# Performance work log

Hardware: AMD Instinct MI355X
Metric: run time of the kernel (lower is better)

Reference implementation:

```python
import jax, jax.numpy as jnp
import numpy as np

B, L, D_MODEL, N_HEAD = 8, 1024, 1024, 16
D_K = D_MODEL // N_HEAD  # 64


def setup_inputs() -> dict:
    key = jax.random.key(0)
    ks = jax.random.split(key, 10)
    scale = 1.0 / np.sqrt(D_MODEL)
    inp = {
        "q": jax.random.normal(ks[0], (B, L, D_MODEL), jnp.float32),
        "k": jax.random.normal(ks[1], (B, L, D_MODEL), jnp.float32),
        "v": jax.random.normal(ks[2], (B, L, D_MODEL), jnp.float32),
        "mask": jax.random.randint(ks[3], (B, L, L), 0, 2, jnp.int32),
        # per-head projection weights stacked: [H, d_model, d_k]
        "Wq": jax.random.normal(ks[4], (N_HEAD, D_MODEL, D_K), jnp.float32) * scale,
        "Wk": jax.random.normal(ks[5], (N_HEAD, D_MODEL, D_K), jnp.float32) * scale,
        "Wv": jax.random.normal(ks[6], (N_HEAD, D_MODEL, D_K), jnp.float32) * scale,
        # output projection (Dense with bias): [d_model, d_model], [d_model]
        "Wo": jax.random.normal(ks[7], (D_MODEL, D_MODEL), jnp.float32) * scale,
        "bo": jnp.zeros((D_MODEL,), jnp.float32),
    }
    return inp


def reference(q, k, v, mask, Wq, Wk, Wv, Wo, bo):
    d_k = Wq.shape[-1]
    # per-head projections (mode=1 per-head Dense, no bias), vectorized over heads
    qs = jnp.einsum('bld,hdk->bhlk', q, Wq)  # [B,H,Lq,d_k]
    ks = jnp.einsum('bld,hdk->bhlk', k, Wk)  # [B,H,Lk,d_k]
    vs = jnp.einsum('bld,hdk->bhlk', v, Wv)  # [B,H,Lk,d_v]
    # scaled dot-product attention: batch_dot(q,k,axes=[2,2]) / sqrt(d_k)
    scores = jnp.einsum('bhqd,bhkd->bhqk', qs, ks) / jnp.sqrt(jnp.float32(d_k))
    # additive mask: -1e9 * (1 - mask), broadcast over heads
    scores = scores + (-1e9 * (1.0 - mask.astype(jnp.float32)))[:, None, :, :]
    attn = jax.nn.softmax(scores, axis=-1)           # [B,H,Lq,Lk] (dropout inactive at inference)
    head = jnp.einsum('bhqk,bhkd->bhqd', attn, vs)   # [B,H,Lq,d_v]
    b, h, lq, dv = head.shape
    # Concatenate heads along feature axis (head index major, as in mode=1 Concatenate)
    head_cat = head.transpose(0, 2, 1, 3).reshape(b, lq, h * dv)
    outputs = head_cat @ Wo + bo                     # [B,Lq,d_model] (dropout inactive)
    # attn heads also concatenated along last axis in mode=1
    attn_cat = attn.transpose(0, 2, 1, 3).reshape(b, lq, h * attn.shape[-1])
    return outputs, attn_cat
```

## Files before the change

### kernel.cpp

```cpp
#include <hip/hip_runtime.h>

typedef _Float16 f16;
typedef _Float16 f16x8 __attribute__((ext_vector_type(8)));
typedef _Float16 f16x4 __attribute__((ext_vector_type(4)));
typedef float f32x4 __attribute__((ext_vector_type(4)));

#define GLOAD_LDS16(g, l) \
    __builtin_amdgcn_global_load_lds((const __attribute__((address_space(1))) void*)(g), \
                                     (__attribute__((address_space(3))) void*)(l), 16, 0, 0)

#define SC_LOG2E 0.180336880f

__global__ __launch_bounds__(256) void cvt3_kernel(const float* __restrict__ q,
        const float* __restrict__ k, const float* __restrict__ v, f16* __restrict__ out) {
    const int z = blockIdx.y;
    const float* src = (z == 0) ? q : (z == 1) ? k : v;
    const size_t i = ((size_t)blockIdx.x * 256 + threadIdx.x) * 8;
    float4 a = *(const float4*)&src[i], b2 = *(const float4*)&src[i + 4];
    f16x8 h;
    h[0] = (f16)a.x; h[1] = (f16)a.y; h[2] = (f16)a.z; h[3] = (f16)a.w;
    h[4] = (f16)b2.x; h[5] = (f16)b2.y; h[6] = (f16)b2.z; h[7] = (f16)b2.w;
    *(f16x8*)&out[(size_t)z * 8388608 + i] = h;
}

__global__ void transpose_w_kernel(const float* __restrict__ Wq, const float* __restrict__ Wk,
        const float* __restrict__ Wv, const float* __restrict__ Wo, f16* __restrict__ out) {
    const int z = blockIdx.y;
    int t = blockIdx.x * 256 + threadIdx.x;
    int n = t >> 10, d = t & 1023;
    float val;
    if (z < 3) {
        const float* W = (z == 0) ? Wq : (z == 1) ? Wk : Wv;
        val = W[((size_t)(n >> 6) * 1024 + d) * 64 + (n & 63)];
    } else {
        val = Wo[(size_t)d * 1024 + n];
    }
    out[(size_t)z * 1048576 + (size_t)n * 1024 + d] = (f16)val;
}

__global__ void maskbits_kernel(const int* __restrict__ mask, unsigned* __restrict__ bits) {
    int t = blockIdx.x * 256 + threadIdx.x;
    const int4* src = (const int4*)mask + (size_t)t * 8;
    unsigned w = 0;
#pragma unroll
    for (int i = 0; i < 8; ++i) {
        int4 v = src[i];
        w |= (v.x != 0 ? 1u : 0u) << (i * 4 + 0);
        w |= (v.y != 0 ? 1u : 0u) << (i * 4 + 1);
        w |= (v.z != 0 ? 1u : 0u) << (i * 4 + 2);
        w |= (v.w != 0 ? 1u : 0u) << (i * 4 + 3);
    }
    bits[t] = w;
}

__global__ __launch_bounds__(256) void proj_kernel(const f16* __restrict__ Ah,
        const f16* __restrict__ Wt, f16* __restrict__ Outp) {
    __shared__ __align__(16) f16 As[128][64];
    __shared__ __align__(16) f16 Bs[128][64];
    const int id = blockIdx.x;
    const int z = id >> 9;
    const int id2 = id & 511;
    const int m0 = ((id2 & 7) * 8 + ((id2 >> 3) & 7)) * 128;
    const int n0 = (id2 >> 6) * 128;
    const f16* A = Ah + (size_t)z * 8388608;
    const f16* Bt = Wt + (size_t)z * 1048576;
    f16* Out = Outp + (size_t)z * 8388608;
    const int tid = threadIdx.x, lane = tid & 63;
    const int w = tid >> 6, wr = w >> 1, wc = w & 1;

    f32x4 acc[4][4];
#pragma unroll
    for (int mi = 0; mi < 4; ++mi)
#pragma unroll
        for (int ni = 0; ni < 4; ++ni) acc[mi][ni] = (f32x4){0.f, 0.f, 0.f, 0.f};

    for (int kt = 0; kt < 16; ++kt) {
        const int k0 = kt * 64;
#pragma unroll
        for (int seg = 0; seg < 4; ++seg) {
            const int ch = seg * 256 + tid, r = ch >> 3, c = ch & 7;
            GLOAD_LDS16(&A[(size_t)(m0 + r) * 1024 + k0 + (c ^ (r & 7)) * 8],
                        (char*)&As[0][0] + (seg * 256 + w * 64) * 16);
            GLOAD_LDS16(&Bt[(size_t)(n0 + r) * 1024 + k0 + (c ^ (r & 7)) * 8],
                        (char*)&Bs[0][0] + (seg * 256 + w * 64) * 16);
        }
        __syncthreads();
#pragma unroll
        for (int ks = 0; ks < 2; ++ks) {
            const int slot = ks * 4 + (lane >> 4);
            f16x8 af[4], bf[4];
#pragma unroll
            for (int mi = 0; mi < 4; ++mi) {
                const int row = wr * 64 + mi * 16 + (lane & 15);
                af[mi] = *(const f16x8*)&As[row][(slot ^ (row & 7)) * 8];
            }
#pragma unroll
            for (int ni = 0; ni < 4; ++ni) {
                const int row = wc * 64 + ni * 16 + (lane & 15);
                bf[ni] = *(const f16x8*)&Bs[row][(slot ^ (row & 7)) * 8];
            }
#pragma unroll
            for (int mi = 0; mi < 4; ++mi)
#pragma unroll
                for (int ni = 0; ni < 4; ++ni)
                    acc[mi][ni] = __builtin_amdgcn_mfma_f32_16x16x32_f16(af[mi], bf[ni], acc[mi][ni], 0, 0, 0);
        }
        __syncthreads();
    }

    const float sc = (z == 0) ? SC_LOG2E : 1.0f;
#pragma unroll
    for (int mi = 0; mi < 4; ++mi)
#pragma unroll
        for (int ni = 0; ni < 4; ++ni) {
            const int row0 = m0 + wr * 64 + mi * 16 + ((lane >> 4) << 2);
            const int col = n0 + wc * 64 + ni * 16 + (lane & 15);
            const int h = col >> 6, kk = col & 63;
            const int b = row0 >> 10, l0 = row0 & 1023;
            if (z < 2) {
#pragma unroll
                for (int r = 0; r < 4; ++r)
                    Out[(((size_t)(b * 16 + h) * 1024) + l0 + r) * 64 + kk] = (f16)(acc[mi][ni][r] * sc);
            } else {
                f16x4 hv;
#pragma unroll
                for (int r = 0; r < 4; ++r) hv[r] = (f16)acc[mi][ni][r];
                *(f16x4*)&Out[((size_t)(b * 16 + h) * 64 + kk) * 1024 + l0] = hv;
            }
        }
}

__global__ __launch_bounds__(256) void out_kernel(const f16* __restrict__ A,
        const f16* __restrict__ Bt, float* __restrict__ O, const float* __restrict__ bias) {
    __shared__ __align__(16) f16 As[128][64];
    __shared__ __align__(16) f16 Bs[128][64];
    const int id2 = blockIdx.x;
    const int m0 = ((id2 & 7) * 8 + ((id2 >> 3) & 7)) * 128;
    const int n0 = (id2 >> 6) * 128;
    const int tid = threadIdx.x, lane = tid & 63;
    const int w = tid >> 6, wr = w >> 1, wc = w & 1;

    f32x4 acc[4][4];
#pragma unroll
    for (int mi = 0; mi < 4; ++mi)
#pragma unroll
        for (int ni = 0; ni < 4; ++ni) acc[mi][ni] = (f32x4){0.f, 0.f, 0.f, 0.f};

    for (int kt = 0; kt < 16; ++kt) {
        const int k0 = kt * 64;
#pragma unroll
        for (int seg = 0; seg < 4; ++seg) {
            const int ch = seg * 256 + tid, r = ch >> 3, c = ch & 7;
            GLOAD_LDS16(&A[(size_t)(m0 + r) * 1024 + k0 + (c ^ (r & 7)) * 8],
                        (char*)&As[0][0] + (seg * 256 + w * 64) * 16);
            GLOAD_LDS16(&Bt[(size_t)(n0 + r) * 1024 + k0 + (c ^ (r & 7)) * 8],
                        (char*)&Bs[0][0] + (seg * 256 + w * 64) * 16);
        }
        __syncthreads();
#pragma unroll
        for (int ks = 0; ks < 2; ++ks) {
            const int slot = ks * 4 + (lane >> 4);
            f16x8 af[4], bf[4];
#pragma unroll
            for (int mi = 0; mi < 4; ++mi) {
                const int row = wr * 64 + mi * 16 + (lane & 15);
                af[mi] = *(const f16x8*)&As[row][(slot ^ (row & 7)) * 8];
            }
#pragma unroll
            for (int ni = 0; ni < 4; ++ni) {
                const int row = wc * 64 + ni * 16 + (lane & 15);
                bf[ni] = *(const f16x8*)&Bs[row][(slot ^ (row & 7)) * 8];
            }
#pragma unroll
            for (int mi = 0; mi < 4; ++mi)
#pragma unroll
                for (int ni = 0; ni < 4; ++ni)
                    acc[mi][ni] = __builtin_amdgcn_mfma_f32_16x16x32_f16(af[mi], bf[ni], acc[mi][ni], 0, 0, 0);
        }
        __syncthreads();
    }

#pragma unroll
    for (int mi = 0; mi < 4; ++mi)
#pragma unroll
        for (int ni = 0; ni < 4; ++ni) {
            const int row0 = m0 + wr * 64 + mi * 16 + ((lane >> 4) << 2);
            const int col = n0 + wc * 64 + ni * 16 + (lane & 15);
            const float bb = bias[col];
#pragma unroll
            for (int r = 0; r < 4; ++r)
                __builtin_nontemporal_store(acc[mi][ni][r] + bb, &O[(size_t)(row0 + r) * 1024 + col]);
        }
}

__global__ __launch_bounds__(256) void attn_fused_kernel(const f16* __restrict__ Qp,
        const f16* __restrict__ Kp, const f16* __restrict__ VpT,
        const unsigned* __restrict__ bits, float* __restrict__ attn, f16* __restrict__ headcat) {
    __shared__ __align__(16) f16 Qs[128][64];
    __shared__ __align__(16) f16 Ks[2][64][64];
    __shared__ __align__(16) f16 Vs[2][64][64];
    __shared__ __align__(16) f16 Ps[128][64];
    __shared__ unsigned bm[128][32];
    const int bh = blockIdx.x & 127, m0 = (blockIdx.x >> 7) * 128;
    const int b = bh >> 4, h = bh & 15;
    const int tid = threadIdx.x, lane = tid & 63, w = tid >> 6;
    const f16* Qbase = Qp + (size_t)bh * 65536;
    const f16* Kbase = Kp + (size_t)bh * 65536;
    const f16* Vbase = VpT + (size_t)bh * 65536;

    auto stageK = [&](int buf, int j) {
#pragma unroll
        for (int seg = 0; seg < 2; ++seg) {
            const int ch = seg * 256 + tid, r = ch >> 3, c = ch & 7;
            GLOAD_LDS16(&Kbase[(size_t)(j * 64 + r) * 64 + (c ^ (r & 7)) * 8],
                        (char*)&Ks[buf][0][0] + (seg * 256 + w * 64) * 16);
        }
    };
    auto stageV = [&](int buf, int j) {
#pragma unroll
        for (int seg = 0; seg < 2; ++seg) {
            const int ch = seg * 256 + tid, r = ch >> 3, c = ch & 7;
            GLOAD_LDS16(&Vbase[(size_t)r * 1024 + j * 64 + (c ^ (r & 7)) * 8],
                        (char*)&Vs[buf][0][0] + (seg * 256 + w * 64) * 16);
        }
    };

#pragma unroll
    for (int seg = 0; seg < 4; ++seg) {
        const int ch = seg * 256 + tid, r = ch >> 3, c = ch & 7;
        GLOAD_LDS16(&Qbase[(size_t)(m0 + r) * 64 + (c ^ (r & 7)) * 8],
                    (char*)&Qs[0][0] + (seg * 256 + w * 64) * 16);
        GLOAD_LDS16((const char*)&bits[((size_t)b * 1024 + m0) * 32] + (size_t)(seg * 256 + tid) * 16,
                    (char*)&bm[0][0] + (seg * 256 + w * 64) * 16);
    }
    stageK(0, 0);
    __syncthreads();

    float lsum[2][4];
#pragma unroll
    for (int mi = 0; mi < 2; ++mi)
#pragma unroll
        for (int r = 0; r < 4; ++r) lsum[mi][r] = 0.f;

    for (int j = 0; j < 16; ++j) {
        if (j < 15) stageK((j + 1) & 1, j + 1);

        f32x4 acc[2][4];
#pragma unroll
        for (int mi = 0; mi < 2; ++mi)
#pragma unroll
            for (int ni = 0; ni < 4; ++ni) acc[mi][ni] = (f32x4){0.f, 0.f, 0.f, 0.f};
#pragma unroll
        for (int ks = 0; ks < 2; ++ks) {
            const int slot = ks * 4 + (lane >> 4);
            f16x8 af[2], bf[4];
#pragma unroll
            for (int mi = 0; mi < 2; ++mi) {
                const int row = w * 32 + mi * 16 + (lane & 15);
                af[mi] = *(const f16x8*)&Qs[row][(slot ^ (row & 7)) * 8];
            }
#pragma unroll
            for (int ni = 0; ni < 4; ++ni) {
                const int row = ni * 16 + (lane & 15);
                bf[ni] = *(const f16x8*)&Ks[j & 1][row][(slot ^ (row & 7)) * 8];
            }
#pragma unroll
            for (int mi = 0; mi < 2; ++mi)
#pragma unroll
                for (int ni = 0; ni < 4; ++ni)
                    acc[mi][ni] = __builtin_amdgcn_mfma_f32_16x16x32_f16(af[mi], bf[ni], acc[mi][ni], 0, 0, 0);
        }

#pragma unroll
        for (int mi = 0; mi < 2; ++mi)
#pragma unroll
            for (int r = 0; r < 4; ++r) {
                const int row = w * 32 + mi * 16 + ((lane >> 4) << 2) + r;
#pragma unroll
                for (int ni = 0; ni < 4; ++ni) {
                    const int col = j * 64 + ni * 16 + (lane & 15);
                    const float p = exp2f(acc[mi][ni][r]);
                    lsum[mi][r] += ((bm[row][col >> 5] >> (col & 31)) & 1) ? p : 0.f;
                }
            }
        __syncthreads();
    }

    stageK(0, 0);
    stageV(0, 0);

    float rl[2][4];
#pragma unroll
    for (int mi = 0; mi < 2; ++mi)
#pragma unroll
        for (int r = 0; r < 4; ++r) {
            float s = lsum[mi][r];
#pragma unroll
            for (int d = 1; d < 16; d <<= 1) s += __shfl_xor(s, d);
            rl[mi][r] = 1.0f / s;
        }

    f32x4 accP[2][4];
#pragma unroll
    for (int mi = 0; mi < 2; ++mi)
#pragma unroll
        for (int ni = 0; ni < 4; ++ni) accP[mi][ni] = (f32x4){0.f, 0.f, 0.f, 0.f};

    float* attnBase = attn + ((size_t)b * 1024 + m0) * 16384 + h * 1024;
    __syncthreads();

    const int st_r0 = tid >> 4;
    const int st_c4 = tid & 15;

    for (int j = 0; j < 16; ++j) {
        if (j < 15) { stageK((j + 1) & 1, j + 1); stageV((j + 1) & 1, j + 1); }

        f32x4 acc[2][4];
#pragma unroll
        for (int mi = 0; mi < 2; ++mi)
#pragma unroll
            for (int ni = 0; ni < 4; ++ni) acc[mi][ni] = (f32x4){0.f, 0.f, 0.f, 0.f};
#pragma unroll
        for (int ks = 0; ks < 2; ++ks) {
            const int slot = ks * 4 + (lane >> 4);
            f16x8 af[2], bf[4];
#pragma unroll
            for (int mi = 0; mi < 2; ++mi) {
                const int row = w * 32 + mi * 16 + (lane & 15);
                af[mi] = *(const f16x8*)&Qs[row][(slot ^ (row & 7)) * 8];
            }
#pragma unroll
            for (int ni = 0; ni < 4; ++ni) {
                const int row = ni * 16 + (lane & 15);
                bf[ni] = *(const f16x8*)&Ks[j & 1][row][(slot ^ (row & 7)) * 8];
            }
#pragma unroll
            for (int mi = 0; mi < 2; ++mi)
#pragma unroll
                for (int ni = 0; ni < 4; ++ni)
                    acc[mi][ni] = __builtin_amdgcn_mfma_f32_16x16x32_f16(af[mi], bf[ni], acc[mi][ni], 0, 0, 0);
        }

#pragma unroll
        for (int mi = 0; mi < 2; ++mi)
#pragma unroll
            for (int r = 0; r < 4; ++r) {
                const int row = w * 32 + mi * 16 + ((lane >> 4) << 2) + r;
                const float ll = rl[mi][r];
#pragma unroll
                for (int ni = 0; ni < 4; ++ni) {
                    const int col = j * 64 + ni * 16 + (lane & 15);
                    float p = exp2f(acc[mi][ni][r]) * ll;
                    p = ((bm[row][col >> 5] >> (col & 31)) & 1) ? p : 0.f;
                    Ps[row][(col & 63) ^ ((row & 7) << 3)] = (f16)p;
                }
            }
        __syncthreads();

#pragma unroll
        for (int i = 0; i < 8; ++i) {
            const int row = st_r0 + 16 * i;
            const f16x4 hv = *(const f16x4*)((const char*)&Ps[row][0] +
                    ((st_c4 >> 1) ^ (row & 7)) * 16 + (st_c4 & 1) * 8);
            f32x4 fv = {(float)hv[0], (float)hv[1], (float)hv[2], (float)hv[3]};
            __builtin_nontemporal_store(fv,
                    (f32x4*)&attnBase[(size_t)row * 16384 + j * 64 + st_c4 * 4]);
        }

#pragma unroll
        for (int ks = 0; ks < 2; ++ks) {
            const int slot = ks * 4 + (lane >> 4);
            f16x8 pf[2], vf[4];
#pragma unroll
            for (int mi = 0; mi < 2; ++mi) {
                const int row = w * 32 + mi * 16 + (lane & 15);
                pf[mi] = *(const f16x8*)&Ps[row][(slot ^ (row & 7)) * 8];
            }
#pragma unroll
            for (int ni = 0; ni < 4; ++ni) {
                const int row = ni * 16 + (lane & 15);
                vf[ni] = *(const f16x8*)&Vs[j & 1][row][(slot ^ (row & 7)) * 8];
            }
#pragma unroll
            for (int mi = 0; mi < 2; ++mi)
#pragma unroll
                for (int ni = 0; ni < 4; ++ni)
                    accP[mi][ni] = __builtin_amdgcn_mfma_f32_16x16x32_f16(pf[mi], vf[ni], accP[mi][ni], 0, 0, 0);
        }
        __syncthreads();
    }

#pragma unroll
    for (int mi = 0; mi < 2; ++mi)
#pragma unroll
        for (int ni = 0; ni < 4; ++ni) {
            const int row0 = m0 + w * 32 + mi * 16 + ((lane >> 4) << 2);
            const int col = ni * 16 + (lane & 15);
#pragma unroll
            for (int r = 0; r < 4; ++r)
                headcat[((size_t)b * 1024 + row0 + r) * 1024 + h * 64 + col] = (f16)accP[mi][ni][r];
        }
}

extern "C" void kernel_launch(void* const* d_in, const int* in_sizes, int n_in,
                              void* d_out, int out_size, void* d_ws, size_t ws_size,
                              hipStream_t stream) {
    const float* q = (const float*)d_in[0];
    const float* k = (const float*)d_in[1];
    const float* v = (const float*)d_in[2];
    const int* mask = (const int*)d_in[3];
    const float* Wq = (const float*)d_in[4];
    const float* Wk = (const float*)d_in[5];
    const float* Wv = (const float*)d_in[6];
    const float* Wo = (const float*)d_in[7];
    const float* bo = (const float*)d_in[8];

    float* out0 = (float*)d_out;
    float* attn = out0 + (size_t)8 * 1024 * 1024;

    char* ws = (char*)d_ws;
    f16* wt   = (f16*)(ws + ((size_t)0 << 20));
    f16* qh   = (f16*)(ws + ((size_t)8 << 20));
    f16* Qp   = (f16*)(ws + ((size_t)56 << 20));
    f16* Kp   = (f16*)(ws + ((size_t)72 << 20));
    f16* VpT  = (f16*)(ws + ((size_t)88 << 20));
    f16* hc   = (f16*)(ws + ((size_t)104 << 20));
    unsigned* bits = (unsigned*)(ws + ((size_t)120 << 20));
    f16* wot  = wt + (size_t)3 * 1048576;

    cvt3_kernel<<<dim3(4096, 3), 256, 0, stream>>>(q, k, v, qh);
    transpose_w_kernel<<<dim3(4096, 4), 256, 0, stream>>>(Wq, Wk, Wv, Wo, wt);
    maskbits_kernel<<<1024, 256, 0, stream>>>(mask, bits);

    proj_kernel<<<1536, 256, 0, stream>>>(qh, wt, Qp);

    attn_fused_kernel<<<1024, 256, 0, stream>>>(Qp, Kp, VpT, bits, attn, hc);

    out_kernel<<<512, 256, 0, stream>>>(hc, wot, out0, bo);
}
```

Measured before the change: 321.2 us.

## Transpose QK MFMA output, use mask-nibble LUTs and packed f16 softmax in attention

The QK^T MFMA operands are swapped so each lane holds four consecutive key columns of one query row. The mask can then be read as a 4-bit nibble from a swizzled bitmask word and expanded through small float/f16 lookup tables, replacing per-element bit tests. Row sums now need only two cross-lane shuffles instead of four per value. Normalisation and masking are done with packed f16 multiplies and written to LDS as 8-byte stores, and V is single-buffered and loaded each iteration. The PV MFMA is moved ahead of the attention-probability global stores. The trade-offs are reduced precision from f16 normalisation and more exposed V load latency without double buffering.

```diff
diff --git a/kernel.cpp b/kernel.cpp
--- a/kernel.cpp
+++ b/kernel.cpp
@@ -3,11 +3,16 @@
 typedef _Float16 f16;
 typedef _Float16 f16x8 __attribute__((ext_vector_type(8)));
 typedef _Float16 f16x4 __attribute__((ext_vector_type(4)));
+typedef _Float16 f16x2 __attribute__((ext_vector_type(2)));
 typedef float f32x4 __attribute__((ext_vector_type(4)));
 
 #define GLOAD_LDS16(g, l) \
     __builtin_amdgcn_global_load_lds((const __attribute__((address_space(1))) void*)(g), \
                                      (__attribute__((address_space(3))) void*)(l), 16, 0, 0)
+
+__device__ __forceinline__ f16x2 cvt_pk_f16(float a, float b) {
+    return __builtin_bit_cast(f16x2, __builtin_amdgcn_cvt_pkrtz(a, b));
+}
 
 #define SC_LOG2E 0.180336880f
 
@@ -198,9 +203,11 @@
         const unsigned* __restrict__ bits, float* __restrict__ attn, f16* __restrict__ headcat) {
     __shared__ __align__(16) f16 Qs[128][64];
     __shared__ __align__(16) f16 Ks[2][64][64];
-    __shared__ __align__(16) f16 Vs[2][64][64];
+    __shared__ __align__(16) f16 Vs[64][64];
     __shared__ __align__(16) f16 Ps[128][64];
     __shared__ unsigned bm[128][32];
+    __shared__ __align__(16) float LUTf[16][4];
+    __shared__ __align__(16) f16 LUTh[16][4];
     const int bh = blockIdx.x & 127, m0 = (blockIdx.x >> 7) * 128;
     const int b = bh >> 4, h = bh & 15;
     const int tid = threadIdx.x, lane = tid & 63, w = tid >> 6;
@@ -216,31 +223,36 @@
                         (char*)&Ks[buf][0][0] + (seg * 256 + w * 64) * 16);
         }
     };
-    auto stageV = [&](int buf, int j) {
+    auto stageV = [&](int j) {
 #pragma unroll
         for (int seg = 0; seg < 2; ++seg) {
             const int ch = seg * 256 + tid, r = ch >> 3, c = ch & 7;
             GLOAD_LDS16(&Vbase[(size_t)r * 1024 + j * 64 + (c ^ (r & 7)) * 8],
-                        (char*)&Vs[buf][0][0] + (seg * 256 + w * 64) * 16);
+                        (char*)&Vs[0][0] + (seg * 256 + w * 64) * 16);
         }
     };
 
+    if (tid < 16) {
+#pragma unroll
+        for (int i = 0; i < 4; ++i) {
+            const float on = ((tid >> i) & 1) ? 1.0f : 0.0f;
+            LUTf[tid][i] = on;
+            LUTh[tid][i] = (f16)on;
+        }
+    }
 #pragma unroll
     for (int seg = 0; seg < 4; ++seg) {
         const int ch = seg * 256 + tid, r = ch >> 3, c = ch & 7;
         GLOAD_LDS16(&Qbase[(size_t)(m0 + r) * 64 + (c ^ (r & 7)) * 8],
                     (char*)&Qs[0][0] + (seg * 256 + w * 64) * 16);
-        GLOAD_LDS16((const char*)&bits[((size_t)b * 1024 + m0) * 32] + (size_t)(seg * 256 + tid) * 16,
+        GLOAD_LDS16((const char*)&bits[((size_t)b * 1024 + m0 + r) * 32] + (c ^ (r & 7)) * 16,
                     (char*)&bm[0][0] + (seg * 256 + w * 64) * 16);
     }
     stageK(0, 0);
     __syncthreads();
 
-    float lsum[2][4];
-#pragma unroll
-    for (int mi = 0; mi < 2; ++mi)
-#pragma unroll
-        for (int r = 0; r < 4; ++r) lsum[mi][r] = 0.f;
+    float lsum[2] = {0.f, 0.f};
+    const int kb0 = (lane >> 4) * 4;
 
     for (int j = 0; j < 16; ++j) {
         if (j < 15) stageK((j + 1) & 1, j + 1);
@@ -268,52 +280,53 @@
             for (int mi = 0; mi < 2; ++mi)
 #pragma unroll
                 for (int ni = 0; ni < 4; ++ni)
-                    acc[mi][ni] = __builtin_amdgcn_mfma_f32_16x16x32_f16(af[mi], bf[ni], acc[mi][ni], 0, 0, 0);
-        }
-
-#pragma unroll
-        for (int mi = 0; mi < 2; ++mi)
-#pragma unroll
-            for (int r = 0; r < 4; ++r) {
-                const int row = w * 32 + mi * 16 + ((lane >> 4) << 2) + r;
-#pragma unroll
-                for (int ni = 0; ni < 4; ++ni) {
-                    const int col = j * 64 + ni * 16 + (lane & 15);
-                    const float p = exp2f(acc[mi][ni][r]);
-                    lsum[mi][r] += ((bm[row][col >> 5] >> (col & 31)) & 1) ? p : 0.f;
-                }
-            }
+                    acc[mi][ni] = __builtin_amdgcn_mfma_f32_16x16x32_f16(bf[ni], af[mi], acc[mi][ni], 0, 0, 0);
+        }
+
+#pragma unroll
+        for (int mi = 0; mi < 2; ++mi) {
+            const int rowm = w * 32 + mi * 16 + (lane & 15);
+            const int swb = (rowm & 7) << 2;
+#pragma unroll
+            for (int ni = 0; ni < 4; ++ni) {
+                const unsigned word = bm[rowm][(2 * j + (ni >> 1)) ^ swb];
+                const unsigned nib = (word >> (((ni & 1) << 4) + kb0)) & 15u;
+                const float4 mf = *(const float4*)&LUTf[nib][0];
+                lsum[mi] = fmaf(exp2f(acc[mi][ni][0]), mf.x, lsum[mi]);
+                lsum[mi] = fmaf(exp2f(acc[mi][ni][1]), mf.y, lsum[mi]);
+                lsum[mi] = fmaf(exp2f(acc[mi][ni][2]), mf.z, lsum[mi]);
+                lsum[mi] = fmaf(exp2f(acc[mi][ni][3]), mf.w, lsum[mi]);
+            }
+        }
         __syncthreads();
     }
 
     stageK(0, 0);
-    stageV(0, 0);
-
-    float rl[2][4];
+
+    f16x2 rlp[2];
+#pragma unroll
+    for (int mi = 0; mi < 2; ++mi) {
+        float s = lsum[mi];
+        s += __shfl_xor(s, 16);
+        s += __shfl_xor(s, 32);
+        const f16 rlh = (f16)(1.0f / s);
+        rlp[mi][0] = rlh; rlp[mi][1] = rlh;
+    }
+
+    f32x4 accP[2][4];
 #pragma unroll
     for (int mi = 0; mi < 2; ++mi)
 #pragma unroll
-        for (int r = 0; r < 4; ++r) {
-            float s = lsum[mi][r];
-#pragma unroll
-            for (int d = 1; d < 16; d <<= 1) s += __shfl_xor(s, d);
-            rl[mi][r] = 1.0f / s;
-        }
-
-    f32x4 accP[2][4];
-#pragma unroll
-    for (int mi = 0; mi < 2; ++mi)
-#pragma unroll
         for (int ni = 0; ni < 4; ++ni) accP[mi][ni] = (f32x4){0.f, 0.f, 0.f, 0.f};
 
     float* attnBase = attn + ((size_t)b * 1024 + m0) * 16384 + h * 1024;
-    __syncthreads();
-
     const int st_r0 = tid >> 4;
     const int st_c4 = tid & 15;
+    __syncthreads();
 
     for (int j = 0; j < 16; ++j) {
-        if (j < 15) { stageK((j + 1) & 1, j + 1); stageV((j + 1) & 1, j + 1); }
+        if (j < 15) stageK((j + 1) & 1, j + 1);
+        stageV(j);
 
         f32x4 acc[2][4];
 #pragma unroll
@@ -338,24 +351,49 @@
             for (int mi = 0; mi < 2; ++mi)
 #pragma unroll
                 for (int ni = 0; ni < 4; ++ni)
-                    acc[mi][ni] = __builtin_amdgcn_mfma_f32_16x16x32_f16(af[mi], bf[ni], acc[mi][ni], 0, 0, 0);
-        }
-
-#pragma unroll
-        for (int mi = 0; mi < 2; ++mi)
-#pragma unroll
-            for (int r = 0; r < 4; ++r) {
-                const int row = w * 32 + mi * 16 + ((lane >> 4) << 2) + r;
-                const float ll = rl[mi][r];
-#pragma unroll
-                for (int ni = 0; ni < 4; ++ni) {
-                    const int col = j * 64 + ni * 16 + (lane & 15);
-                    float p = exp2f(acc[mi][ni][r]) * ll;
-                    p = ((bm[row][col >> 5] >> (col & 31)) & 1) ? p : 0.f;
-                    Ps[row][(col & 63) ^ ((row & 7) << 3)] = (f16)p;
-                }
-            }
-        __syncthreads();
+                    acc[mi][ni] = __builtin_amdgcn_mfma_f32_16x16x32_f16(bf[ni], af[mi], acc[mi][ni], 0, 0, 0);
+        }
+
+#pragma unroll
+        for (int mi = 0; mi < 2; ++mi) {
+            const int rowm = w * 32 + mi * 16 + (lane & 15);
+            const int swb = (rowm & 7) << 2;
+            const int swp = (rowm & 7) << 3;
+#pragma unroll
+            for (int ni = 0; ni < 4; ++ni) {
+                const unsigned word = bm[rowm][(2 * j + (ni >> 1)) ^ swb];
+                const unsigned nib = (word >> (((ni & 1) << 4) + kb0)) & 15u;
+                const f16x4 mh = *(const f16x4*)&LUTh[nib][0];
+                f16x2 p01 = cvt_pk_f16(exp2f(acc[mi][ni][0]), exp2f(acc[mi][ni][1]));
+                f16x2 p23 = cvt_pk_f16(exp2f(acc[mi][ni][2]), exp2f(acc[mi][ni][3]));
+                p01 = p01 * (f16x2){mh[0], mh[1]} * rlp[mi];
+                p23 = p23 * (f16x2){mh[2], mh[3]} * rlp[mi];
+                f16x4 pw; pw[0] = p01[0]; pw[1] = p01[1]; pw[2] = p23[0]; pw[3] = p23[1];
+                *(f16x4*)&Ps[rowm][(ni * 16 + kb0) ^ swp] = pw;
+            }
+        }
+        __syncthreads();
+
+#pragma unroll
+        for (int ks = 0; ks < 2; ++ks) {
+            const int slot = ks * 4 + (lane >> 4);
+            f16x8 pf[2], vf[4];
+#pragma unroll
+            for (int mi = 0; mi < 2; ++mi) {
+                const int row = w * 32 + mi * 16 + (lane & 15);
+                pf[mi] = *(const f16x8*)&Ps[row][(slot ^ (row & 7)) * 8];
+            }
+#pragma unroll
+            for (int ni = 0; ni < 4; ++ni) {
+                const int row = ni * 16 + (lane & 15);
+                vf[ni] = *(const f16x8*)&Vs[row][(slot ^ (row & 7)) * 8];
+            }
+#pragma unroll
+            for (int mi = 0; mi < 2; ++mi)
+#pragma unroll
+                for (int ni = 0; ni < 4; ++ni)
+                    accP[mi][ni] = __builtin_amdgcn_mfma_f32_16x16x32_f16(pf[mi], vf[ni], accP[mi][ni], 0, 0, 0);
+        }
 
 #pragma unroll
         for (int i = 0; i < 8; ++i) {
@@ -365,27 +403,6 @@
             f32x4 fv = {(float)hv[0], (float)hv[1], (float)hv[2], (float)hv[3]};
             __builtin_nontemporal_store(fv,
                     (f32x4*)&attnBase[(size_t)row * 16384 + j * 64 + st_c4 * 4]);
-        }
-
-#pragma unroll
-        for (int ks = 0; ks < 2; ++ks) {
-            const int slot = ks * 4 + (lane >> 4);
-            f16x8 pf[2], vf[4];
-#pragma unroll
-            for (int mi = 0; mi < 2; ++mi) {
-                const int row = w * 32 + mi * 16 + (lane & 15);
-                pf[mi] = *(const f16x8*)&Ps[row][(slot ^ (row & 7)) * 8];
-            }
-#pragma unroll
-            for (int ni = 0; ni < 4; ++ni) {
-                const int row = ni * 16 + (lane & 15);
-                vf[ni] = *(const f16x8*)&Vs[j & 1][row][(slot ^ (row & 7)) * 8];
-            }
-#pragma unroll
-            for (int mi = 0; mi < 2; ++mi)
-#pragma unroll
-                for (int ni = 0; ni < 4; ++ni)
-                    accP[mi][ni] = __builtin_amdgcn_mfma_f32_16x16x32_f16(pf[mi], vf[ni], accP[mi][ni], 0, 0, 0);
         }
         __syncthreads();
     }
```

Result: faster. 298.9 us (-7.0%).
